# Kernel tuning notes

Hardware: AMD Instinct MI355X
Metric: run time of the kernel (lower is better)

Reference implementation:

```python
import jax, jax.numpy as jnp
import numpy as np

NUM_BINS = 256


def _equalize_channel(chan):
    # chan: (P,) int32 pixel values in [0, 255]. PIL/torchvision-style equalize.
    hist = jnp.zeros(NUM_BINS, jnp.float32).at[chan].add(1.0)
    total = hist.sum()
    # value of the last nonzero histogram bin (excluded from step computation)
    nz = hist > 0
    last_idx = (NUM_BINS - 1) - jnp.argmax(nz[::-1])
    last = hist[last_idx]
    step = jnp.floor((total - last) / 255.0)
    cum = jnpp_cumsum = jnp.cumsum(hist)
    lut = jnp.floor((cum + jnp.floor(step / 2.0)) / jnp.maximum(step, 1.0))
    # shift right by one (pad a leading 0, drop last) and clamp to [0,255]
    lut = jnp.clip(jnp.concatenate([jnp.zeros(1, jnp.float32), lut[:-1]]), 0.0, 255.0)
    ident = jnp.arange(NUM_BINS, dtype=jnp.float32)
    lut = jnp.where(step == 0, ident, lut)  # step==0 -> identity mapping
    return lut[chan]


def _equalize(x):
    # x: (N, C, H, W) float, pixel values -> uint8 semantics
    N, C, H, W = x.shape
    xi = jnp.clip(x, 0, 255).astype(jnp.int32).reshape(N * C, H * W)
    out = jax.vmap(_equalize_channel)(xi)  # (N*C, H*W) float32
    return out.reshape(N, C, H, W).astype(x.dtype)


def setup_inputs() -> dict:
    key = jax.random.key(0)
    x = jax.random.uniform(key, (64, 3, 512, 512), dtype=jnp.float32) * 255.0
    magnitude = 5
    return {"x": x, "magnitude": magnitude}


def reference(x, magnitude):
    # magnitude is unused in the original forward (Equalize ignores it)
    return _equalize(x)
```

## Files before the change

kernel.cpp:

```cpp
#include <hip/hip_runtime.h>

#define NBINS 256
#define NCHAN 192
#define BPC 8
#define TPB 256
#define NCOPY 16
#define F4_PER_CHAN 65536
#define F4_PER_BLK (F4_PER_CHAN / BPC)

typedef float f4 __attribute__((ext_vector_type(4)));


__global__ __launch_bounds__(TPB) void eq_hist_pack(const float* __restrict__ x,
                                                    unsigned* __restrict__ packed,
                                                    int* __restrict__ partials) {
    __shared__ int lh[NBINS * NCOPY];
    const int tid = threadIdx.x;
    const int cp  = (tid & 63) >> 2;

    for (int i = tid; i < NBINS * NCOPY; i += TPB) lh[i] = 0;
    __syncthreads();

    const size_t base = (size_t)blockIdx.x * F4_PER_BLK;
    const f4* bx = (const f4*)x + base;
    unsigned* bp = packed + base;

    for (int i = tid; i < F4_PER_BLK; i += TPB) {
        f4 v = __builtin_nontemporal_load(&bx[i]);
        int a = (int)fminf(fmaxf(v.x, 0.f), 255.f);
        int b = (int)fminf(fmaxf(v.y, 0.f), 255.f);
        int c = (int)fminf(fmaxf(v.z, 0.f), 255.f);
        int d = (int)fminf(fmaxf(v.w, 0.f), 255.f);
        bp[i] = (unsigned)(a | (b << 8) | (c << 16) | (d << 24));
        atomicAdd(&lh[(a << 4) + cp], 1);
        atomicAdd(&lh[(b << 4) + cp], 1);
        atomicAdd(&lh[(c << 4) + cp], 1);
        atomicAdd(&lh[(d << 4) + cp], 1);
    }
    __syncthreads();

    int s = 0;
    #pragma unroll
    for (int k = 0; k < NCOPY; ++k) s += lh[(tid << 4) + ((tid + k) & 15)];
    partials[blockIdx.x * NBINS + tid] = s;
}

__global__ __launch_bounds__(TPB) void eq_lut(const int* __restrict__ partials,
                                              float* __restrict__ lut) {
    __shared__ int scan[NBINS];
    __shared__ int s_last_idx, s_last;
    const int chan = blockIdx.x;
    const int tid  = threadIdx.x;

    int h = 0;
    #pragma unroll
    for (int b = 0; b < BPC; ++b)
        h += partials[(chan * BPC + b) * NBINS + tid];
    scan[tid] = h;
    if (tid == 0) s_last_idx = 0;
    __syncthreads();
    if (h > 0) atomicMax(&s_last_idx, tid);

    for (int off = 1; off < NBINS; off <<= 1) {
        int t = (tid >= off) ? scan[tid - off] : 0;
        __syncthreads();
        scan[tid] += t;
        __syncthreads();
    }
    if (tid == s_last_idx) s_last = h;
    __syncthreads();

    const int total = scan[NBINS - 1];
    const int step  = (total - s_last) / 255;

    float lutv;
    if (step == 0)      lutv = (float)tid;
    else if (tid == 0)  lutv = 0.f;
    else {
        int l = (scan[tid - 1] + (step >> 1)) / step;
        lutv = (float)(l < 255 ? l : 255);
    }
    lut[chan * NBINS + tid] = lutv;
}

__global__ __launch_bounds__(TPB) void eq_apply(const unsigned* __restrict__ packed,
                                                float* __restrict__ out,
                                                const float* __restrict__ lut) {
    __shared__ float slut[NBINS * NCOPY];
    const int chan = blockIdx.x / BPC;
    const int tid  = threadIdx.x;
    const int cp   = (tid & 63) >> 2;

    const float lv = lut[chan * NBINS + tid];
    #pragma unroll
    for (int k = 0; k < NCOPY; ++k) slut[(tid << 4) + ((tid + k) & 15)] = lv;
    __syncthreads();

    const size_t base = (size_t)blockIdx.x * F4_PER_BLK;
    const unsigned* bp = packed + base;
    f4* bo = (f4*)out + base;

    for (int i = tid; i < F4_PER_BLK; i += TPB) {
        unsigned p = bp[i];
        f4 o;
        o.x = slut[(int)((p & 255u) << 4) + cp];
        o.y = slut[(int)(((p >> 8) & 255u) << 4) + cp];
        o.z = slut[(int)(((p >> 16) & 255u) << 4) + cp];
        o.w = slut[(int)((p >> 24) << 4) + cp];
        __builtin_nontemporal_store(o, &bo[i]);
    }
}

extern "C" void kernel_launch(void* const* d_in, const int* in_sizes, int n_in,
                              void* d_out, int out_size, void* d_ws, size_t ws_size,
                              hipStream_t stream) {
    const float* x = (const float*)d_in[0];
    float* out = (float*)d_out;

    unsigned* packed = (unsigned*)d_ws;
    int* partials = (int*)d_ws + (size_t)NCHAN * F4_PER_CHAN;
    float* lut = (float*)(partials + (size_t)NCHAN * BPC * NBINS);

    eq_hist_pack<<<NCHAN * BPC, TPB, 0, stream>>>(x, packed, partials);
    eq_lut<<<NCHAN, TPB, 0, stream>>>(partials, lut);
    eq_apply<<<NCHAN * BPC, TPB, 0, stream>>>(packed, out, lut);
}
```

Baseline: 342.0 us.

## Fuse histogram, LUT, and apply into one kernel with inter-block flags

Merges the three kernels into a single kernel where each thread keeps its packed pixel bytes in registers, blocks of a channel publish partial histograms and spin on a per-channel atomic counter, then each block builds the LUT and writes outputs. This removes the global write and reread of the packed intermediate and two kernel launches. It relies on all blocks of a channel being co-resident (launch bounds set for occupancy), risking deadlock or stalls if scheduling differs, and adds a small flag-reset kernel.

```diff
diff --git a/kernel.cpp b/kernel.cpp
--- a/kernel.cpp
+++ b/kernel.cpp
@@ -4,34 +4,41 @@
 #define NCHAN 192
 #define BPC 8
 #define TPB 256
+#define PPT 32
 #define NCOPY 16
-#define F4_PER_CHAN 65536
-#define F4_PER_BLK (F4_PER_CHAN / BPC)
+#define F4_PER_BLK (TPB * PPT)
 
 typedef float f4 __attribute__((ext_vector_type(4)));
 
+__global__ __launch_bounds__(TPB, 6) void eq_fused(const float* __restrict__ x,
+                                                   float* __restrict__ out,
+                                                   int* __restrict__ partials,
+                                                   int* __restrict__ done) {
+    __shared__ int lh[NBINS * NCOPY];
+    __shared__ int scan[NBINS];
+    __shared__ int s_last_idx, s_last;
 
-__global__ __launch_bounds__(TPB) void eq_hist_pack(const float* __restrict__ x,
-                                                    unsigned* __restrict__ packed,
-                                                    int* __restrict__ partials) {
-    __shared__ int lh[NBINS * NCOPY];
-    const int tid = threadIdx.x;
-    const int cp  = (tid & 63) >> 2;
+    const int bid  = blockIdx.x;
+    const int chan = bid / BPC;
+    const int tid  = threadIdx.x;
+    const int cp   = (tid & 63) >> 2;
 
     for (int i = tid; i < NBINS * NCOPY; i += TPB) lh[i] = 0;
+    if (tid == 0) s_last_idx = 0;
     __syncthreads();
 
-    const size_t base = (size_t)blockIdx.x * F4_PER_BLK;
+    const size_t base = (size_t)bid * F4_PER_BLK;
     const f4* bx = (const f4*)x + base;
-    unsigned* bp = packed + base;
 
-    for (int i = tid; i < F4_PER_BLK; i += TPB) {
-        f4 v = __builtin_nontemporal_load(&bx[i]);
+    unsigned px[PPT];
+    #pragma unroll
+    for (int k = 0; k < PPT; ++k) {
+        f4 v = __builtin_nontemporal_load(&bx[tid + k * TPB]);
         int a = (int)fminf(fmaxf(v.x, 0.f), 255.f);
         int b = (int)fminf(fmaxf(v.y, 0.f), 255.f);
         int c = (int)fminf(fmaxf(v.z, 0.f), 255.f);
         int d = (int)fminf(fmaxf(v.w, 0.f), 255.f);
-        bp[i] = (unsigned)(a | (b << 8) | (c << 16) | (d << 24));
+        px[k] = (unsigned)(a | (b << 8) | (c << 16) | (d << 24));
         atomicAdd(&lh[(a << 4) + cp], 1);
         atomicAdd(&lh[(b << 4) + cp], 1);
         atomicAdd(&lh[(c << 4) + cp], 1);
@@ -42,22 +49,24 @@
     int s = 0;
     #pragma unroll
     for (int k = 0; k < NCOPY; ++k) s += lh[(tid << 4) + ((tid + k) & 15)];
-    partials[blockIdx.x * NBINS + tid] = s;
-}
+    partials[bid * NBINS + tid] = s;
+    __threadfence();
+    __syncthreads();
+    if (tid == 0)
+        __hip_atomic_fetch_add(&done[chan], 1, __ATOMIC_RELEASE, __HIP_MEMORY_SCOPE_AGENT);
 
-__global__ __launch_bounds__(TPB) void eq_lut(const int* __restrict__ partials,
-                                              float* __restrict__ lut) {
-    __shared__ int scan[NBINS];
-    __shared__ int s_last_idx, s_last;
-    const int chan = blockIdx.x;
-    const int tid  = threadIdx.x;
+    if (tid == 0) {
+        while (__hip_atomic_load(&done[chan], __ATOMIC_ACQUIRE, __HIP_MEMORY_SCOPE_AGENT) < BPC)
+            __builtin_amdgcn_s_sleep(8);
+    }
+    __syncthreads();
 
     int h = 0;
     #pragma unroll
     for (int b = 0; b < BPC; ++b)
-        h += partials[(chan * BPC + b) * NBINS + tid];
+        h += __hip_atomic_load(&partials[(chan * BPC + b) * NBINS + tid],
+                               __ATOMIC_RELAXED, __HIP_MEMORY_SCOPE_AGENT);
     scan[tid] = h;
-    if (tid == 0) s_last_idx = 0;
     __syncthreads();
     if (h > 0) atomicMax(&s_last_idx, tid);
 
@@ -72,7 +81,6 @@
 
     const int total = scan[NBINS - 1];
     const int step  = (total - s_last) / 255;
-
     float lutv;
     if (step == 0)      lutv = (float)tid;
     else if (tid == 0)  lutv = 0.f;
@@ -80,35 +88,26 @@
         int l = (scan[tid - 1] + (step >> 1)) / step;
         lutv = (float)(l < 255 ? l : 255);
     }
-    lut[chan * NBINS + tid] = lutv;
-}
-
-__global__ __launch_bounds__(TPB) void eq_apply(const unsigned* __restrict__ packed,
-                                                float* __restrict__ out,
-                                                const float* __restrict__ lut) {
-    __shared__ float slut[NBINS * NCOPY];
-    const int chan = blockIdx.x / BPC;
-    const int tid  = threadIdx.x;
-    const int cp   = (tid & 63) >> 2;
-
-    const float lv = lut[chan * NBINS + tid];
+    float* slut = (float*)lh;
     #pragma unroll
-    for (int k = 0; k < NCOPY; ++k) slut[(tid << 4) + ((tid + k) & 15)] = lv;
+    for (int k = 0; k < NCOPY; ++k) slut[(tid << 4) + ((tid + k) & 15)] = lutv;
     __syncthreads();
 
-    const size_t base = (size_t)blockIdx.x * F4_PER_BLK;
-    const unsigned* bp = packed + base;
     f4* bo = (f4*)out + base;
-
-    for (int i = tid; i < F4_PER_BLK; i += TPB) {
-        unsigned p = bp[i];
+    #pragma unroll
+    for (int k = 0; k < PPT; ++k) {
+        unsigned p = px[k];
         f4 o;
         o.x = slut[(int)((p & 255u) << 4) + cp];
         o.y = slut[(int)(((p >> 8) & 255u) << 4) + cp];
         o.z = slut[(int)(((p >> 16) & 255u) << 4) + cp];
         o.w = slut[(int)((p >> 24) << 4) + cp];
-        __builtin_nontemporal_store(o, &bo[i]);
+        __builtin_nontemporal_store(o, &bo[tid + k * TPB]);
     }
+}
+
+__global__ void eq_zero_flags(int* __restrict__ done) {
+    if (threadIdx.x < NCHAN) done[threadIdx.x] = 0;
 }
 
 extern "C" void kernel_launch(void* const* d_in, const int* in_sizes, int n_in,
@@ -117,11 +116,9 @@
     const float* x = (const float*)d_in[0];
     float* out = (float*)d_out;
 
-    unsigned* packed = (unsigned*)d_ws;
-    int* partials = (int*)d_ws + (size_t)NCHAN * F4_PER_CHAN;
-    float* lut = (float*)(partials + (size_t)NCHAN * BPC * NBINS);
+    int* partials = (int*)d_ws;
+    int* done = partials + (size_t)NCHAN * BPC * NBINS;
 
-    eq_hist_pack<<<NCHAN * BPC, TPB, 0, stream>>>(x, packed, partials);
-    eq_lut<<<NCHAN, TPB, 0, stream>>>(partials, lut);
-    eq_apply<<<NCHAN * BPC, TPB, 0, stream>>>(packed, out, lut);
+    eq_zero_flags<<<1, TPB, 0, stream>>>(done);
+    eq_fused<<<NCHAN * BPC, TPB, 0, stream>>>(x, out, partials, done);
 }
```

Measured after the change: 584.8 us. +71.0%, slower.
